# Kernel tuning notes

Measured on AMD Instinct MI355X. Metric: run time of the kernel, lower is better.

## Reference

```python
import jax, jax.numpy as jnp
import numpy as np

MAGNITUDE = 9
PROB = 0.5
WARP_STRENGTH = MAGNITUDE * 0.3 / 9.0  # = 0.3


def _notaknot_matrix(S):
    # System for second derivatives M of a cubic spline on uniform grid h=1
    # (scipy CubicSpline default bc_type='not-a-knot').
    A = np.zeros((S, S), dtype=np.float32)
    i = np.arange(1, S - 1)
    A[i, i - 1] = 1.0
    A[i, i] = 4.0
    A[i, i + 1] = 1.0
    # not-a-knot: third derivative continuous at x1 and x_{S-2}
    A[0, 0], A[0, 1], A[0, 2] = 1.0, -2.0, 1.0
    A[-1, -3], A[-1, -2], A[-1, -1] = 1.0, -2.0, 1.0
    return A


def setup_inputs() -> dict:
    key = jax.random.key(0)
    k1, k2, k3 = jax.random.split(key, 3)
    B, C, S = 128, 64, 4096
    x = jax.random.normal(k1, (B, C, S), dtype=jnp.float32)
    # per-sample scale ~ U(1 - warp_strength, 1 + warp_strength)
    scale = (1.0 - WARP_STRENGTH) + 2.0 * WARP_STRENGTH * jax.random.uniform(k2, (B,), dtype=jnp.float32)
    # per-sample apply decision: rand < prob
    apply_mask = jax.random.uniform(k3, (B,)) < PROB
    return {"x": x, "scale": scale, "apply_mask": apply_mask}


def reference(x, scale, apply_mask):
    B, C, S = x.shape
    A = jnp.asarray(_notaknot_matrix(S))  # (S, S), fixed uniform-grid system

    # --- fit not-a-knot cubic splines for all B*C signals at once ---
    y = x.reshape(B * C, S)
    rhs = jnp.zeros_like(y).at[:, 1:-1].set(
        6.0 * (y[:, :-2] - 2.0 * y[:, 1:-1] + y[:, 2:])
    )  # not-a-knot rows have rhs 0
    M = jnp.linalg.solve(A, rhs.T).T.reshape(B, C, S)  # second derivatives

    # --- warped evaluation points (shared across channels of a sample) ---
    grid = jnp.arange(S, dtype=x.dtype)
    w = jnp.clip(grid[None, :] * scale[:, None], 0.0, S - 1)  # (B, S)
    idx = jnp.clip(jnp.floor(w).astype(jnp.int32), 0, S - 2)  # interval index
    t = (w - idx.astype(x.dtype))[:, None, :]                 # (B, 1, S)

    idx3 = jnp.broadcast_to(idx[:, None, :], (B, C, S))
    y0 = jnp.take_along_axis(x, idx3, axis=2)
    y1 = jnp.take_along_axis(x, idx3 + 1, axis=2)
    M0 = jnp.take_along_axis(M, idx3, axis=2)
    M1 = jnp.take_along_axis(M, idx3 + 1, axis=2)

    # s(t) = y0 + b t + c t^2 + d t^3 on each unit interval (h = 1)
    b = (y1 - y0) - (2.0 * M0 + M1) / 6.0
    c = M0 / 2.0
    d = (M1 - M0) / 6.0
    warped = y0 + t * (b + t * (c + t * d))

    return jnp.where(apply_mask[:, None, None], warped, x)
```

## Files before the change

kernel.cpp:

```cpp
#include <hip/hip_runtime.h>
#include <math.h>


#define SLEN 4096
#define WRAD 8
#define BLK  256

typedef float f32x4 __attribute__((ext_vector_type(4)));

__device__ __attribute__((noinline))
f32x4 edge_eval(const float* __restrict__ sy, int j0, float sc)
{
    const float log2r = -1.8999686269529532f;
    const float r = 0.26794919243112270f;
    float G[WRAD + 1];
    G[0] = 0.28867513459481287f;
    #pragma unroll
    for (int k = 1; k <= WRAD; ++k) G[k] = -G[k - 1] * r;

    const float M1  = sy[0]        - 2.0f * sy[1]        + sy[2];
    const float MS2 = sy[SLEN - 3] - 2.0f * sy[SLEN - 2] + sy[SLEN - 1];

    float v1 = 0.0f, vS2 = 0.0f;
    #pragma unroll
    for (int k = 1; k <= WRAD; ++k) {
        const int ja = 1 + k;
        float fa = 6.0f * (sy[ja - 1] - 2.0f * sy[ja] + sy[ja + 1]);
        if (ja == 2) fa -= M1;
        v1 += G[k] * fa;
        const int jb = SLEN - 2 - k;
        float fb = 6.0f * (sy[jb - 1] - 2.0f * sy[jb] + sy[jb + 1]);
        if (jb == SLEN - 3) fb -= MS2;
        vS2 += G[k] * fb;
    }

    auto Mconv = [&](int i) -> float {
        float acc = 0.0f;
        #pragma unroll
        for (int k = -WRAD; k <= WRAD; ++k) {
            const int j = i + k;
            float fj = 0.0f;
            if (j >= 2 && j <= SLEN - 3) {
                fj = 6.0f * (sy[j - 1] - 2.0f * sy[j] + sy[j + 1]);
                if (j == 2)        fj -= M1;
                if (j == SLEN - 3) fj -= MS2;
            }
            acc += G[k < 0 ? -k : k] * fj;
        }
        if (i <= 34) {
            float cc = v1 * exp2f((float)(i - 1) * log2r);
            acc += (i & 1) ? -cc : cc;
        }
        if (i >= SLEN - 36) {
            float cc = vS2 * exp2f((float)(SLEN - 2 - i) * log2r);
            acc += (i & 1) ? cc : -cc;
        }
        return acc;
    };
    auto Mfull = [&](int i) -> float {
        if (i == 1)        return M1;
        if (i == SLEN - 2) return MS2;
        if (i == 0)        return 2.0f * M1  - Mconv(2);
        if (i == SLEN - 1) return 2.0f * MS2 - Mconv(SLEN - 3);
        return Mconv(i);
    };

    f32x4 rv;
    float w0 = fminf((float)j0 * sc, (float)(SLEN - 1));
    int  id0 = (int)w0; if (id0 > SLEN - 2) id0 = SLEN - 2;
    if (id0 == SLEN - 2) {
        const float m0 = MS2;
        const float m1 = 2.0f * MS2 - Mconv(SLEN - 3);
        const float y0 = sy[SLEN - 2], y1 = sy[SLEN - 1];
        const float bb = (y1 - y0) - (2.0f * m0 + m1) * (1.0f / 6.0f);
        const float cf = 0.5f * m0;
        const float dd = (m1 - m0) * (1.0f / 6.0f);
        #pragma unroll
        for (int e = 0; e < 4; ++e) {
            float w  = fminf((float)(j0 + e) * sc, (float)(SLEN - 1));
            float tt = w - (float)(SLEN - 2);
            rv[e] = y0 + tt * (bb + tt * (cf + tt * dd));
        }
        return rv;
    }
    #pragma unroll
    for (int e = 0; e < 4; ++e) {
        float w  = fminf((float)(j0 + e) * sc, (float)(SLEN - 1));
        int  id  = (int)w; if (id > SLEN - 2) id = SLEN - 2;
        const float tt = w - (float)id;
        const float m0 = Mfull(id);
        const float m1 = Mfull(id + 1);
        const float y0 = sy[id], y1 = sy[id + 1];
        const float bb = (y1 - y0) - (2.0f * m0 + m1) * (1.0f / 6.0f);
        const float cf = 0.5f * m0;
        const float dd = (m1 - m0) * (1.0f / 6.0f);
        rv[e] = y0 + tt * (bb + tt * (cf + tt * dd));
    }
    return rv;
}

__global__ __launch_bounds__(BLK, 5) void time_warp_kernel(
    const float* __restrict__ x,
    const float* __restrict__ scale,
    const int*   __restrict__ apply_mask,
    float* __restrict__ out,
    int C)
{
    __shared__ float sy[SLEN];

    const int bid = blockIdx.x;
    const int b   = bid / C;
    const int t   = threadIdx.x;
    const float* __restrict__ xin = x   + (size_t)bid * SLEN;
    float*       __restrict__ o   = out + (size_t)bid * SLEN;

    if (apply_mask[b] == 0) {
        const f32x4* __restrict__ xi4 = (const f32x4*)xin;
        f32x4*       __restrict__ o4  = (f32x4*)o;
        #pragma unroll
        for (int k = 0; k < 4; ++k) {
            f32x4 v = xi4[t + BLK * k];
            __builtin_nontemporal_store(v, &o4[t + BLK * k]);
        }
        return;
    }

    {
        const float4* __restrict__ xi4 = (const float4*)xin;
        #pragma unroll
        for (int k = 0; k < 4; ++k)
            *(float4*)&sy[4 * (t + BLK * k)] = xi4[t + BLK * k];
    }
    __syncthreads();

    const float sc = scale[b];

    const float r = 0.26794919243112270f;
    float G[WRAD + 1];
    G[0] = 0.28867513459481287f;
    #pragma unroll
    for (int k = 1; k <= WRAD; ++k) G[k] = -G[k - 1] * r;
    float Hh[WRAD + 2];
    Hh[0] = 12.0f * (G[1] - G[0]);
    #pragma unroll
    for (int k = 1; k < WRAD; ++k) Hh[k] = 6.0f * (G[k - 1] - 2.0f * G[k] + G[k + 1]);
    Hh[WRAD]     = 6.0f * (G[WRAD - 1] - 2.0f * G[WRAD]);
    Hh[WRAD + 1] = 6.0f * G[WRAD];

    #pragma unroll
    for (int s = 0; s < 4; ++s) {
        const int j0 = 4 * t + 1024 * s;
        const int idx0 = (int)fminf((float)j0 * sc, (float)(SLEN - 1));
        f32x4 res;

        if (idx0 >= 35 && idx0 <= SLEN - 42) {
            const float* __restrict__ wp = &sy[idx0 - 9];
            float wv[24];
            #pragma unroll
            for (int m = 0; m < 24; ++m) wv[m] = wp[m];

            float Ms[6];
            #pragma unroll
            for (int ii = 0; ii < 6; ++ii) {
                float acc = Hh[0] * wv[9 + ii];
                #pragma unroll
                for (int k = 1; k <= WRAD + 1; ++k)
                    acc += Hh[k] * (wv[9 + ii - k] + wv[9 + ii + k]);
                Ms[ii] = acc;
            }

            #pragma unroll
            for (int e = 0; e < 4; ++e) {
                const float w  = (float)(j0 + e) * sc;
                const int   id = (int)w;
                const float tt = w - (float)id;
                const int   d  = id - idx0;
                float m0 = Ms[0], m1 = Ms[1];
                if (d >= 1) { m0 = Ms[1]; m1 = Ms[2]; }
                if (d >= 2) { m0 = Ms[2]; m1 = Ms[3]; }
                if (d >= 3) { m0 = Ms[3]; m1 = Ms[4]; }
                if (d >= 4) { m0 = Ms[4]; m1 = Ms[5]; }
                const float y0 = sy[id], y1 = sy[id + 1];
                const float bb = (y1 - y0) - (2.0f * m0 + m1) * (1.0f / 6.0f);
                const float cf = 0.5f * m0;
                const float dd = (m1 - m0) * (1.0f / 6.0f);
                res[e] = y0 + tt * (bb + tt * (cf + tt * dd));
            }
        } else {
            res = edge_eval(sy, j0, sc);
        }

        __builtin_nontemporal_store(res, (f32x4*)&o[j0]);
    }
}

extern "C" void kernel_launch(void* const* d_in, const int* in_sizes, int n_in,
                              void* d_out, int out_size, void* d_ws, size_t ws_size,
                              hipStream_t stream) {
    const float* x     = (const float*)d_in[0];
    const float* scale = (const float*)d_in[1];
    const int*   mask  = (const int*)d_in[2];
    float*       out   = (float*)d_out;

    const int B     = in_sizes[1];
    const int total = in_sizes[0];
    const int C     = total / (B * SLEN);
    const int nblk  = B * C;

    time_warp_kernel<<<nblk, BLK, 0, stream>>>(x, scale, mask, out, C);
}
```

Measured before the change: 259.2 us.

## Parallelize spline evaluation over source intervals instead of output samples

Each thread now owns a group of four source intervals and computes exactly the five second derivatives it needs. It then writes every output sample whose warped position falls in those intervals, using inverse-scale start indices found with exact correction loops. This removes the per-output interval selection and the redundant sixth convolution. Outputs past the clamp point are filled with the last sample. The cost is data-dependent inner loops and scalar nontemporal stores in place of vectorized float4 stores, which may hurt write coalescing and add divergence.

```diff
diff --git a/kernel.cpp b/kernel.cpp
--- a/kernel.cpp
+++ b/kernel.cpp
@@ -8,9 +8,23 @@
 
 typedef float f32x4 __attribute__((ext_vector_type(4)));
 
+__device__ __forceinline__ int jstart_f(int i, float sc, float inv) {
+    const float fi = (float)i;
+    int js = (int)ceilf(fi * inv);
+    if (js < 0) js = 0;
+    while ((float)js * sc < fi) ++js;
+    while (js > 0 && (float)(js - 1) * sc >= fi) --js;
+    return js;
+}
+
 __device__ __attribute__((noinline))
-f32x4 edge_eval(const float* __restrict__ sy, int j0, float sc)
+void edge_group(const float* __restrict__ sy, float* __restrict__ o,
+                int i0, float sc, float inv, int jcap)
 {
+    int a  = jstart_f(i0, sc, inv);     if (a  > jcap) a  = jcap;
+    int a4 = jstart_f(i0 + 4, sc, inv); if (a4 > jcap) a4 = jcap;
+    if (a >= a4) return;
+
     const float log2r = -1.8999686269529532f;
     const float r = 0.26794919243112270f;
     float G[WRAD + 1];
@@ -65,38 +79,31 @@
         return Mconv(i);
     };
 
-    f32x4 rv;
-    float w0 = fminf((float)j0 * sc, (float)(SLEN - 1));
-    int  id0 = (int)w0; if (id0 > SLEN - 2) id0 = SLEN - 2;
-    if (id0 == SLEN - 2) {
-        const float m0 = MS2;
-        const float m1 = 2.0f * MS2 - Mconv(SLEN - 3);
-        const float y0 = sy[SLEN - 2], y1 = sy[SLEN - 1];
+    float Ms[5];
+    #pragma unroll
+    for (int k = 0; k < 5; ++k) {
+        int ik = i0 + k; if (ik > SLEN - 1) ik = SLEN - 1;
+        Ms[k] = Mfull(ik);
+    }
+
+    #pragma unroll
+    for (int k = 0; k < 4; ++k) {
+        int bnd = jstart_f(i0 + k + 1, sc, inv); if (bnd > jcap) bnd = jcap;
+        const int iy0 = i0 + k;
+        const int iy1 = (iy0 + 1 > SLEN - 1) ? SLEN - 1 : iy0 + 1;
+        const float y0 = sy[iy0 > SLEN - 1 ? SLEN - 1 : iy0];
+        const float y1 = sy[iy1];
+        const float m0 = Ms[k], m1 = Ms[k + 1];
         const float bb = (y1 - y0) - (2.0f * m0 + m1) * (1.0f / 6.0f);
         const float cf = 0.5f * m0;
         const float dd = (m1 - m0) * (1.0f / 6.0f);
-        #pragma unroll
-        for (int e = 0; e < 4; ++e) {
-            float w  = fminf((float)(j0 + e) * sc, (float)(SLEN - 1));
-            float tt = w - (float)(SLEN - 2);
-            rv[e] = y0 + tt * (bb + tt * (cf + tt * dd));
-        }
-        return rv;
-    }
-    #pragma unroll
-    for (int e = 0; e < 4; ++e) {
-        float w  = fminf((float)(j0 + e) * sc, (float)(SLEN - 1));
-        int  id  = (int)w; if (id > SLEN - 2) id = SLEN - 2;
-        const float tt = w - (float)id;
-        const float m0 = Mfull(id);
-        const float m1 = Mfull(id + 1);
-        const float y0 = sy[id], y1 = sy[id + 1];
-        const float bb = (y1 - y0) - (2.0f * m0 + m1) * (1.0f / 6.0f);
-        const float cf = 0.5f * m0;
-        const float dd = (m1 - m0) * (1.0f / 6.0f);
-        rv[e] = y0 + tt * (bb + tt * (cf + tt * dd));
-    }
-    return rv;
+        for (int j = a; j < bnd; ++j) {
+            const float w  = (float)j * sc;
+            const float tt = w - (float)(i0 + k);
+            __builtin_nontemporal_store(y0 + tt * (bb + tt * (cf + tt * dd)), &o[j]);
+        }
+        a = bnd;
+    }
 }
 
 __global__ __launch_bounds__(BLK, 5) void time_warp_kernel(
@@ -133,7 +140,10 @@
     }
     __syncthreads();
 
-    const float sc = scale[b];
+    const float sc  = scale[b];
+    const float inv = 1.0f / sc;
+    int jcap = jstart_f(SLEN - 1, sc, inv);
+    if (jcap > SLEN) jcap = SLEN;
 
     const float r = 0.26794919243112270f;
     float G[WRAD + 1];
@@ -149,48 +159,53 @@
 
     #pragma unroll
     for (int s = 0; s < 4; ++s) {
-        const int j0 = 4 * t + 1024 * s;
-        const int idx0 = (int)fminf((float)j0 * sc, (float)(SLEN - 1));
-        f32x4 res;
-
-        if (idx0 >= 35 && idx0 <= SLEN - 42) {
-            const float* __restrict__ wp = &sy[idx0 - 9];
-            float wv[24];
+        const int i0 = 4 * t + 1024 * s;
+        if (i0 >= 36 && i0 <= SLEN - 44) {
+            int a  = jstart_f(i0, sc, inv);     if (a  > jcap) a  = jcap;
+            int a4 = jstart_f(i0 + 4, sc, inv); if (a4 > jcap) a4 = jcap;
+            if (a >= a4) continue;
+
+            float wv[28];
             #pragma unroll
-            for (int m = 0; m < 24; ++m) wv[m] = wp[m];
-
-            float Ms[6];
+            for (int m = 0; m < 7; ++m)
+                *(float4*)&wv[4 * m] = *(const float4*)&sy[i0 - 12 + 4 * m];
+
+            float Ms[5];
             #pragma unroll
-            for (int ii = 0; ii < 6; ++ii) {
-                float acc = Hh[0] * wv[9 + ii];
+            for (int ii = 0; ii < 5; ++ii) {
+                float acc = Hh[0] * wv[12 + ii];
                 #pragma unroll
                 for (int k = 1; k <= WRAD + 1; ++k)
-                    acc += Hh[k] * (wv[9 + ii - k] + wv[9 + ii + k]);
+                    acc += Hh[k] * (wv[12 + ii - k] + wv[12 + ii + k]);
                 Ms[ii] = acc;
             }
 
             #pragma unroll
-            for (int e = 0; e < 4; ++e) {
-                const float w  = (float)(j0 + e) * sc;
-                const int   id = (int)w;
-                const float tt = w - (float)id;
-                const int   d  = id - idx0;
-                float m0 = Ms[0], m1 = Ms[1];
-                if (d >= 1) { m0 = Ms[1]; m1 = Ms[2]; }
-                if (d >= 2) { m0 = Ms[2]; m1 = Ms[3]; }
-                if (d >= 3) { m0 = Ms[3]; m1 = Ms[4]; }
-                if (d >= 4) { m0 = Ms[4]; m1 = Ms[5]; }
-                const float y0 = sy[id], y1 = sy[id + 1];
+            for (int k = 0; k < 4; ++k) {
+                int bnd;
+                if (k == 3) bnd = a4;
+                else { bnd = jstart_f(i0 + k + 1, sc, inv); if (bnd > jcap) bnd = jcap; }
+                const float y0 = wv[12 + k], y1 = wv[13 + k];
+                const float m0 = Ms[k], m1 = Ms[k + 1];
                 const float bb = (y1 - y0) - (2.0f * m0 + m1) * (1.0f / 6.0f);
                 const float cf = 0.5f * m0;
                 const float dd = (m1 - m0) * (1.0f / 6.0f);
-                res[e] = y0 + tt * (bb + tt * (cf + tt * dd));
+                for (int j = a; j < bnd; ++j) {
+                    const float w  = (float)j * sc;
+                    const float tt = w - (float)(i0 + k);
+                    __builtin_nontemporal_store(y0 + tt * (bb + tt * (cf + tt * dd)), &o[j]);
+                }
+                a = bnd;
             }
         } else {
-            res = edge_eval(sy, j0, sc);
-        }
-
-        __builtin_nontemporal_store(res, (f32x4*)&o[j0]);
+            edge_group(sy, o, i0, sc, inv, jcap);
+        }
+    }
+
+    if (jcap < SLEN) {
+        const float yS1 = sy[SLEN - 1];
+        for (int j = jcap + t; j < SLEN; j += BLK)
+            __builtin_nontemporal_store(yS1, &o[j]);
     }
 }
 
```

Result: slower. 335.2 us (+29.3%).
